# Kernel tuning notes

Hardware: AMD Instinct MI355X
Metric: run time of the kernel (lower is better)

Reference implementation:

```python
import jax, jax.numpy as jnp
import numpy as np

NUM_NODES = 100000
NUM_EDGES = 3_200_000
WALKS_PER_NODE = 4
WALK_LENGTH = 8
SKIP_FIRST = True


def setup_inputs() -> dict:
    key = jax.random.key(0)
    k1, k2, k3 = jax.random.split(key, 3)
    edge_index = jax.random.randint(k1, (2, NUM_EDGES), 0, NUM_NODES, dtype=jnp.int32)
    edge_weight = jax.random.uniform(k2, (NUM_EDGES,), dtype=jnp.float32)
    # one uniform per walker per step; S = NUM_NODES * WALKS_PER_NODE
    rand_unif = jax.random.uniform(k3, (NUM_NODES * WALKS_PER_NODE, WALK_LENGTH), dtype=jnp.float32)
    return {"edge_index": edge_index, "edge_weight": edge_weight, "rand_unif": rand_unif}


def _random_walk_edges(edge_index, rand_unif):
    """Returns added [2, S*L] edges (root -> walked node), int dtype."""
    row, col = edge_index[0], edge_index[1]
    # is_sorted=False path: sort edges by source to build CSR
    order = jnp.argsort(row)
    row_s = row[order]
    col_s = col[order]
    deg = jax.ops.segment_sum(jnp.ones_like(row_s), row_s, num_segments=NUM_NODES)  # [N]
    rowptr = jnp.concatenate([jnp.zeros((1,), deg.dtype), jnp.cumsum(deg)])  # [N+1]
    # start = all nodes, repeated walks_per_node times
    start = jnp.tile(jnp.arange(NUM_NODES, dtype=row.dtype), WALKS_PER_NODE)  # [S]

    def step(cur, u):
        d = deg[cur]  # [S]
        off = jnp.minimum((u * d.astype(u.dtype)).astype(cur.dtype), jnp.maximum(d - 1, 0))
        nxt = jnp.where(d > 0, col_s[rowptr[cur] + off], cur)  # stay if isolated
        return nxt, nxt

    _, walks = jax.lax.scan(step, start, rand_unif.T)  # [L_total, S]
    walks = walks.T  # [S, WALK_LENGTH] == n_id[:, 1:]
    k = 1 if SKIP_FIRST else 0  # skip_first drops the first-hop node (n_id[:, 2:])
    targets = walks[:, k:]  # [S, L]
    L = targets.shape[1]
    roots = jnp.broadcast_to(start[:, None], (start.shape[0], L))
    return jnp.stack([roots.reshape(-1), targets.reshape(-1)])  # [2, S*L]


def reference(edge_index, edge_weight, rand_unif):
    added = _random_walk_edges(edge_index, rand_unif)
    out_edge_index = jnp.concatenate([edge_index, added], axis=1)
    added_w = jnp.ones((added.shape[1],), edge_weight.dtype)
    out_edge_weight = jnp.concatenate([edge_weight, added_w])
    return out_edge_index, out_edge_weight
```

## Files before the change

### kernel.cpp

```cpp
#include <hip/hip_runtime.h>

#define ARW_N_NODES   100000
#define ARW_N_EDGES   3200000
#define ARW_N_WALKERS 400000
#define ARW_WLEN      8
#define ARW_LOUT      7
#define ARW_ROW_LEN   6000000
#define ARW_OUT_ELEMS 18000000

#define ARW_NB    196
#define ARW_NT    3125
#define ARW_TP    3136
#define ARW_TILE  1024

#define ARW_HT    0
#define ARW_BT    700000
#define ARW_TOT   1350000
#define ARW_CB    1360000
#define ARW_PD    1400000
#define ARW_P     6000000
#define ARW_COLS  12000000

__global__ void AddRandomWalkEdge_16896401342869_kernel() {}

__global__ __launch_bounds__(1024) void arw16896_thist(const int* __restrict__ row,
                                                       int* __restrict__ s) {
    __shared__ int h[256];
    int tid = threadIdx.x;
    if (tid < 256) h[tid] = 0;
    __syncthreads();
    atomicAdd(&h[row[blockIdx.x * ARW_TILE + tid] >> 9], 1);
    __syncthreads();
    if (tid < ARW_NB) s[ARW_HT + tid * ARW_TP + blockIdx.x] = h[tid];
}

__global__ __launch_bounds__(1024) void arw16896_btot(int* __restrict__ s) {
    __shared__ int wsum[16];
    int b = blockIdx.x, tid = threadIdx.x, lane = tid & 63, wid = tid >> 6;
    int acc = 0;
    for (int t = tid; t < ARW_NT; t += 1024) acc += s[ARW_HT + b * ARW_TP + t];
    #pragma unroll
    for (int off = 32; off > 0; off >>= 1) acc += __shfl_down(acc, off, 64);
    if (lane == 0) wsum[wid] = acc;
    __syncthreads();
    if (tid == 0) {
        int a = 0;
        #pragma unroll
        for (int w = 0; w < 16; w++) a += wsum[w];
        s[ARW_TOT + b] = a;
    }
}

__global__ __launch_bounds__(256) void arw16896_bbase(int* __restrict__ s) {
    __shared__ int sm[256];
    int tid = threadIdx.x;
    int v = (tid < ARW_NB) ? s[ARW_TOT + tid] : 0;
    sm[tid] = v;
    __syncthreads();
    for (int off = 1; off < 256; off <<= 1) {
        int x = 0;
        if (tid >= off) x = sm[tid - off];
        __syncthreads();
        sm[tid] += x;
        __syncthreads();
    }
    if (tid < ARW_NB) s[ARW_CB + tid] = sm[tid] - v;
}

__global__ __launch_bounds__(1024) void arw16896_bscan2(int* __restrict__ s) {
    __shared__ int wsum[16];
    int b = blockIdx.x, tid = threadIdx.x, lane = tid & 63, wid = tid >> 6;
    int carry = s[ARW_CB + b];
    for (int c0 = 0; c0 < ARW_NT; c0 += 1024) {
        int t = c0 + tid;
        int v = (t < ARW_NT) ? s[ARW_HT + b * ARW_TP + t] : 0;
        int sv = v;
        #pragma unroll
        for (int off = 1; off < 64; off <<= 1) {
            int x = __shfl_up(sv, off, 64);
            if (lane >= off) sv += x;
        }
        if (lane == 63) wsum[wid] = sv;
        __syncthreads();
        int pre = 0, tot = 0;
        #pragma unroll
        for (int w = 0; w < 16; w++) {
            int x = wsum[w];
            if (w < wid) pre += x;
            tot += x;
        }
        if (t < ARW_NT) s[ARW_BT + b * ARW_TP + t] = carry + pre + sv - v;
        carry += tot;
        __syncthreads();
    }
}

__global__ __launch_bounds__(1024) void arw16896_part(const int* __restrict__ row,
                                                      const int* __restrict__ col,
                                                      int* __restrict__ s) {
    __shared__ unsigned W[16 * 256];
    int tid  = threadIdx.x;
    int wave = tid >> 6, lane = tid & 63;
    int e = blockIdx.x * ARW_TILE + tid;
    int r = row[e], cv = col[e];
    int b = r >> 9;
    W[tid] = 0; W[tid + 1024] = 0; W[tid + 2048] = 0; W[tid + 3072] = 0;
    __syncthreads();
    unsigned long long mask = ~0ULL;
    #pragma unroll
    for (int bit = 0; bit < 8; bit++) {
        unsigned long long bal = __ballot((b >> bit) & 1);
        mask &= ((b >> bit) & 1) ? bal : ~bal;
    }
    int rankw = __popcll(mask & ((1ULL << lane) - 1ULL));
    W[wave * 256 + b] = (unsigned)__popcll(mask);
    __syncthreads();
    int cross = 0;
    for (int w2 = 0; w2 < 16; w2++) {
        if (w2 >= wave) break;
        cross += (int)W[w2 * 256 + b];
    }
    int base = s[ARW_BT + b * ARW_TP + blockIdx.x];
    s[ARW_P + base + cross + rankw] = ((r & 511) << 17) | cv;
}

__global__ __launch_bounds__(1024) void arw16896_pass2(int* __restrict__ s) {
    __shared__ unsigned W[16 * 512];
    __shared__ int hist[512], pref[512], runc[512];
    int tid = threadIdx.x, lane = tid & 63, wave = tid >> 6;
    int b = blockIdx.x;
    int start = s[ARW_BT + b * ARW_TP];
    int end   = (b == ARW_NB - 1) ? ARW_N_EDGES : s[ARW_BT + (b + 1) * ARW_TP];
    int cnt = end - start;
    int rows0 = b << 9;
    int nrows = ARW_N_NODES - rows0; if (nrows > 512) nrows = 512;

    if (tid < 512) hist[tid] = 0;
    __syncthreads();
    for (int k = tid; k < cnt; k += 1024)
        atomicAdd(&hist[(unsigned)s[ARW_P + start + k] >> 17], 1);
    __syncthreads();
    if (tid < 512) pref[tid] = hist[tid];
    __syncthreads();
    for (int off = 1; off < 512; off <<= 1) {
        int x = 0;
        if (tid < 512 && tid >= off) x = pref[tid - off];
        __syncthreads();
        if (tid < 512) pref[tid] += x;
        __syncthreads();
    }
    if (tid < 512) runc[tid] = 0;
    if (tid < nrows) {
        unsigned deg = (unsigned)hist[tid];
        unsigned rp  = (unsigned)(start + pref[tid] - hist[tid]);
        s[ARW_PD + rows0 + tid] = (int)((rp << 10) | deg);
    }
    __syncthreads();

    for (int c0 = 0; c0 < cnt; c0 += 1024) {
        int k = c0 + tid;
        int valid = (k < cnt) ? 1 : 0;
        unsigned p = valid ? (unsigned)s[ARW_P + start + k] : 0u;
        unsigned lr = p >> 17;
        #pragma unroll
        for (int j = 0; j < 8; j++) W[tid + j * 1024] = 0;
        __syncthreads();
        unsigned long long mask = ~0ULL;
        #pragma unroll
        for (int bit = 0; bit < 9; bit++) {
            unsigned long long bal = __ballot((lr >> bit) & 1u);
            mask &= ((lr >> bit) & 1u) ? bal : ~bal;
        }
        mask &= __ballot(valid);
        int rankw = __popcll(mask & ((1ULL << lane) - 1ULL));
        if (valid) W[wave * 512 + lr] = (unsigned)__popcll(mask);
        __syncthreads();
        if (valid) {
            int cross = 0;
            for (int w2 = 0; w2 < 16; w2++) {
                if (w2 >= wave) break;
                cross += (int)W[w2 * 512 + lr];
            }
            int pos = start + (pref[lr] - hist[lr]) + runc[lr] + cross + rankw;
            s[ARW_COLS + pos] = (int)(p & 0x1FFFFu);
        }
        __syncthreads();
        if (tid < 512) {
            int a = 0;
            #pragma unroll
            for (int w = 0; w < 16; w++) a += (int)W[w * 512 + tid];
            runc[tid] += a;
        }
        __syncthreads();
    }
}

__global__ __launch_bounds__(256) void arw16896_walk(const float* __restrict__ ru,
                                                     const int* __restrict__ s,
                                                     float* __restrict__ o) {
    __shared__ float tg[4 * 256 * ARW_LOUT];
    int tid = threadIdx.x;
    int v = blockIdx.x * 256 + tid;
    if (v < ARW_N_NODES) {
        float uu[4][8];
        int cur[4];
        #pragma unroll
        for (int k = 0; k < 4; k++) {
            const float4* rp4 = (const float4*)(ru + (size_t)(v + k * ARW_N_NODES) * 8);
            float4 ra = rp4[0], rb = rp4[1];
            uu[k][0] = ra.x; uu[k][1] = ra.y; uu[k][2] = ra.z; uu[k][3] = ra.w;
            uu[k][4] = rb.x; uu[k][5] = rb.y; uu[k][6] = rb.z; uu[k][7] = rb.w;
        }
        unsigned pd0 = (unsigned)s[ARW_PD + v];
        int d0  = (int)(pd0 & 1023u);
        int rp0 = (int)(pd0 >> 10);
        #pragma unroll
        for (int k = 0; k < 4; k++) {
            int off = (int)(uu[k][0] * (float)d0);
            if (off > d0 - 1) off = d0 - 1;
            int nxt = s[ARW_COLS + rp0 + off];
            cur[k] = (d0 > 0) ? nxt : v;
        }
        #pragma unroll
        for (int t = 1; t < ARW_WLEN; t++) {
            unsigned pdk[4];
            #pragma unroll
            for (int k = 0; k < 4; k++) pdk[k] = (unsigned)s[ARW_PD + cur[k]];
            #pragma unroll
            for (int k = 0; k < 4; k++) {
                int d = (int)(pdk[k] & 1023u);
                int off = (int)(uu[k][t] * (float)d);
                if (off > d - 1) off = d - 1;
                int nxt = s[ARW_COLS + (int)(pdk[k] >> 10) + off];
                cur[k] = (d > 0) ? nxt : cur[k];
                tg[k * (256 * ARW_LOUT) + tid * ARW_LOUT + (t - 1)] = (float)cur[k];
            }
        }
    }
    __syncthreads();
    int blkN = ARW_N_NODES - blockIdx.x * 256;
    if (blkN > 256) blkN = 256;
    int valid = blkN * ARW_LOUT;
    #pragma unroll
    for (int k = 0; k < 4; k++) {
        int base = ARW_ROW_LEN + ARW_N_EDGES +
                   (k * ARW_N_NODES + blockIdx.x * 256) * ARW_LOUT;
        for (int j = tid; j < valid; j += 256)
            o[base + j] = tg[k * (256 * ARW_LOUT) + j];
    }
}

__global__ __launch_bounds__(256) void arw16896_asm(const int* __restrict__ ei,
                                                    const float* __restrict__ wgt,
                                                    float* __restrict__ o) {
    int i4 = blockIdx.x * blockDim.x + threadIdx.x;
    if (i4 < ARW_N_EDGES / 4) {
        int4 r0 = ((const int4*)ei)[i4];
        int4 r1 = ((const int4*)(ei + ARW_N_EDGES))[i4];
        float4 wv = ((const float4*)wgt)[i4];
        ((float4*)o)[i4] = make_float4((float)r0.x, (float)r0.y, (float)r0.z, (float)r0.w);
        ((float4*)(o + ARW_ROW_LEN))[i4] =
            make_float4((float)r1.x, (float)r1.y, (float)r1.z, (float)r1.w);
        ((float4*)(o + 2 * ARW_ROW_LEN))[i4] = wv;
    }
    if (i4 < (ARW_N_WALKERS * ARW_LOUT) / 4) {
        int i = i4 * 4;
        float4 r;
        r.x = (float)(((i    ) / ARW_LOUT) % ARW_N_NODES);
        r.y = (float)(((i + 1) / ARW_LOUT) % ARW_N_NODES);
        r.z = (float)(((i + 2) / ARW_LOUT) % ARW_N_NODES);
        r.w = (float)(((i + 3) / ARW_LOUT) % ARW_N_NODES);
        ((float4*)(o + ARW_N_EDGES))[i4] = r;
        ((float4*)(o + 2 * ARW_ROW_LEN + ARW_N_EDGES))[i4] = make_float4(1.f, 1.f, 1.f, 1.f);
    }
}

extern "C" void kernel_launch(void* const* d_in, const int* in_sizes, int n_in,
                              void* d_out, int out_size, void* d_ws, size_t ws_size,
                              hipStream_t stream) {
    const int*   ei  = (const int*)d_in[0];
    const float* wgt = (const float*)d_in[1];
    const float* ru  = (const float*)d_in[2];
    int*   s = (int*)d_out;
    float* o = (float*)d_out;
    const int* row = ei;
    const int* col = ei + ARW_N_EDGES;

    arw16896_thist <<<ARW_NT, 1024, 0, stream>>>(row, s);
    arw16896_btot  <<<ARW_NB, 1024, 0, stream>>>(s);
    arw16896_bbase <<<1, 256, 0, stream>>>(s);
    arw16896_bscan2<<<ARW_NB, 1024, 0, stream>>>(s);
    arw16896_part  <<<ARW_NT, 1024, 0, stream>>>(row, col, s);
    arw16896_pass2 <<<ARW_NB, 1024, 0, stream>>>(s);
    arw16896_walk  <<<(ARW_N_NODES + 255) / 256, 256, 0, stream>>>(ru, s, o);
    arw16896_asm   <<<(ARW_N_EDGES / 4 + 255) / 256, 256, 0, stream>>>(ei, wgt, o);
}
```

Before: 247.2 us.

## Use 256 row buckets, batch histogram tiles per block, shrink walk blocks

Row buckets change from 512 rows each to 392 rows each, giving 256 buckets, so the bucket-sort stages launch 256 blocks instead of 196 and fill more CUs. The histogram kernel now processes 25 tiles per block with per-tile shared histograms, which cuts its launch count. The walk kernel drops from 256-thread to 64-thread blocks, giving more blocks so the latency-bound random gathers spread better across CUs. Workspace offsets are moved to fit the larger histogram table, and the division by 392 costs more than the old shift.

```diff
diff --git a/kernel.cpp b/kernel.cpp
--- a/kernel.cpp
+++ b/kernel.cpp
@@ -8,16 +8,18 @@
 #define ARW_ROW_LEN   6000000
 #define ARW_OUT_ELEMS 18000000
 
-#define ARW_NB    196
+#define ARW_NB    256
+#define ARW_RPB   392
 #define ARW_NT    3125
 #define ARW_TP    3136
 #define ARW_TILE  1024
+#define ARW_TPB   25
 
 #define ARW_HT    0
-#define ARW_BT    700000
-#define ARW_TOT   1350000
-#define ARW_CB    1360000
-#define ARW_PD    1400000
+#define ARW_BT    900000
+#define ARW_TOT   1750000
+#define ARW_CB    1760000
+#define ARW_PD    1800000
 #define ARW_P     6000000
 #define ARW_COLS  12000000
 
@@ -25,13 +27,19 @@
 
 __global__ __launch_bounds__(1024) void arw16896_thist(const int* __restrict__ row,
                                                        int* __restrict__ s) {
-    __shared__ int h[256];
+    __shared__ int h[ARW_TPB * 256];
     int tid = threadIdx.x;
-    if (tid < 256) h[tid] = 0;
-    __syncthreads();
-    atomicAdd(&h[row[blockIdx.x * ARW_TILE + tid] >> 9], 1);
-    __syncthreads();
-    if (tid < ARW_NB) s[ARW_HT + tid * ARW_TP + blockIdx.x] = h[tid];
+    for (int x = tid; x < ARW_TPB * 256; x += 1024) h[x] = 0;
+    __syncthreads();
+    int base_e = blockIdx.x * (ARW_TPB * ARW_TILE) + tid;
+    #pragma unroll
+    for (int j = 0; j < ARW_TPB; j++)
+        atomicAdd(&h[j * 256 + (row[base_e + j * 1024] / ARW_RPB)], 1);
+    __syncthreads();
+    for (int x = tid; x < ARW_TPB * ARW_NB; x += 1024) {
+        int b = x / ARW_TPB, j = x % ARW_TPB;
+        s[ARW_HT + b * ARW_TP + blockIdx.x * ARW_TPB + j] = h[j * 256 + b];
+    }
 }
 
 __global__ __launch_bounds__(1024) void arw16896_btot(int* __restrict__ s) {
@@ -54,7 +62,7 @@
 __global__ __launch_bounds__(256) void arw16896_bbase(int* __restrict__ s) {
     __shared__ int sm[256];
     int tid = threadIdx.x;
-    int v = (tid < ARW_NB) ? s[ARW_TOT + tid] : 0;
+    int v = s[ARW_TOT + tid];
     sm[tid] = v;
     __syncthreads();
     for (int off = 1; off < 256; off <<= 1) {
@@ -64,7 +72,7 @@
         sm[tid] += x;
         __syncthreads();
     }
-    if (tid < ARW_NB) s[ARW_CB + tid] = sm[tid] - v;
+    s[ARW_CB + tid] = sm[tid] - v;
 }
 
 __global__ __launch_bounds__(1024) void arw16896_bscan2(int* __restrict__ s) {
@@ -103,7 +111,8 @@
     int wave = tid >> 6, lane = tid & 63;
     int e = blockIdx.x * ARW_TILE + tid;
     int r = row[e], cv = col[e];
-    int b = r >> 9;
+    int b = r / ARW_RPB;
+    int lr = r - b * ARW_RPB;
     W[tid] = 0; W[tid + 1024] = 0; W[tid + 2048] = 0; W[tid + 3072] = 0;
     __syncthreads();
     unsigned long long mask = ~0ULL;
@@ -121,7 +130,7 @@
         cross += (int)W[w2 * 256 + b];
     }
     int base = s[ARW_BT + b * ARW_TP + blockIdx.x];
-    s[ARW_P + base + cross + rankw] = ((r & 511) << 17) | cv;
+    s[ARW_P + base + cross + rankw] = (lr << 17) | cv;
 }
 
 __global__ __launch_bounds__(1024) void arw16896_pass2(int* __restrict__ s) {
@@ -132,8 +141,8 @@
     int start = s[ARW_BT + b * ARW_TP];
     int end   = (b == ARW_NB - 1) ? ARW_N_EDGES : s[ARW_BT + (b + 1) * ARW_TP];
     int cnt = end - start;
-    int rows0 = b << 9;
-    int nrows = ARW_N_NODES - rows0; if (nrows > 512) nrows = 512;
+    int rows0 = b * ARW_RPB;
+    int nrows = ARW_N_NODES - rows0; if (nrows > ARW_RPB) nrows = ARW_RPB;
 
     if (tid < 512) hist[tid] = 0;
     __syncthreads();
@@ -195,12 +204,12 @@
     }
 }
 
-__global__ __launch_bounds__(256) void arw16896_walk(const float* __restrict__ ru,
-                                                     const int* __restrict__ s,
-                                                     float* __restrict__ o) {
-    __shared__ float tg[4 * 256 * ARW_LOUT];
+__global__ __launch_bounds__(64) void arw16896_walk(const float* __restrict__ ru,
+                                                    const int* __restrict__ s,
+                                                    float* __restrict__ o) {
+    __shared__ float tg[4 * 64 * ARW_LOUT];
     int tid = threadIdx.x;
-    int v = blockIdx.x * 256 + tid;
+    int v = blockIdx.x * 64 + tid;
     if (v < ARW_N_NODES) {
         float uu[4][8];
         int cur[4];
@@ -233,20 +242,20 @@
                 if (off > d - 1) off = d - 1;
                 int nxt = s[ARW_COLS + (int)(pdk[k] >> 10) + off];
                 cur[k] = (d > 0) ? nxt : cur[k];
-                tg[k * (256 * ARW_LOUT) + tid * ARW_LOUT + (t - 1)] = (float)cur[k];
+                tg[k * (64 * ARW_LOUT) + tid * ARW_LOUT + (t - 1)] = (float)cur[k];
             }
         }
     }
     __syncthreads();
-    int blkN = ARW_N_NODES - blockIdx.x * 256;
-    if (blkN > 256) blkN = 256;
+    int blkN = ARW_N_NODES - blockIdx.x * 64;
+    if (blkN > 64) blkN = 64;
     int valid = blkN * ARW_LOUT;
     #pragma unroll
     for (int k = 0; k < 4; k++) {
         int base = ARW_ROW_LEN + ARW_N_EDGES +
-                   (k * ARW_N_NODES + blockIdx.x * 256) * ARW_LOUT;
-        for (int j = tid; j < valid; j += 256)
-            o[base + j] = tg[k * (256 * ARW_LOUT) + j];
+                   (k * ARW_N_NODES + blockIdx.x * 64) * ARW_LOUT;
+        for (int j = tid; j < valid; j += 64)
+            o[base + j] = tg[k * (64 * ARW_LOUT) + j];
     }
 }
 
@@ -286,12 +295,12 @@
     const int* row = ei;
     const int* col = ei + ARW_N_EDGES;
 
-    arw16896_thist <<<ARW_NT, 1024, 0, stream>>>(row, s);
+    arw16896_thist <<<ARW_NT / ARW_TPB, 1024, 0, stream>>>(row, s);
     arw16896_btot  <<<ARW_NB, 1024, 0, stream>>>(s);
     arw16896_bbase <<<1, 256, 0, stream>>>(s);
     arw16896_bscan2<<<ARW_NB, 1024, 0, stream>>>(s);
     arw16896_part  <<<ARW_NT, 1024, 0, stream>>>(row, col, s);
     arw16896_pass2 <<<ARW_NB, 1024, 0, stream>>>(s);
-    arw16896_walk  <<<(ARW_N_NODES + 255) / 256, 256, 0, stream>>>(ru, s, o);
+    arw16896_walk  <<<(ARW_N_NODES + 63) / 64, 64, 0, stream>>>(ru, s, o);
     arw16896_asm   <<<(ARW_N_EDGES / 4 + 255) / 256, 256, 0, stream>>>(ei, wgt, o);
 }
```

Result: slower. 252.8 us (+2.2%).
